# Kernel optimization log

Measured on AMD Instinct MI355X. Metric: run time of the kernel, lower is better.

The kernel has to match this reference:

```python
import jax, jax.numpy as jnp
import numpy as np

B, L, D, H = 8, 2048, 128, 128
MASK_VALUE = -1e30


def setup_inputs() -> dict:
    key = jax.random.key(0)
    ks = jax.random.split(key, 5)
    return {
        "query": jax.random.normal(ks[0], (B, L, D), dtype=jnp.float32),
        "key": jax.random.normal(ks[1], (B, L, D), dtype=jnp.float32),
        "value": jax.random.normal(ks[2], (B, L, D), dtype=jnp.float32),
        "mask": jnp.ones((B, L), dtype=jnp.float32),
        "Wq": jax.random.normal(ks[3], (D, H), dtype=jnp.float32) * (1.0 / np.sqrt(D)),
        "Wk": jax.random.normal(ks[4], (D, H), dtype=jnp.float32) * (1.0 / np.sqrt(D)),
    }


def reference(query, key, value, mask, Wq, Wk):
    # q: [B,Lq,H], k: [B,Lk,H]
    q = jnp.einsum("bqd,dh->bqh", query, Wq)
    k = jnp.einsum("bkd,dh->bkh", key, Wk)
    # unscaled scores [B,Lq,Lk]
    A = jnp.einsum("bqh,bkh->bqk", q, k)
    m = mask[:, None, :]  # [B,1,Lk]
    A = m * A + (1.0 - m) * MASK_VALUE
    # inference path: no dropout (learning_phase False)
    A = jax.nn.softmax(A, axis=-1)
    return jnp.einsum("bqk,bkd->bqd", A, value)
```

## Files before the change

kernel.cpp:

```cpp
#include <hip/hip_runtime.h>

#define NB 8
#define NL 2048
#define ND 128
#define NH 128
#define MASKVAL (-1e30f)

typedef __attribute__((ext_vector_type(8))) short short8;
typedef __attribute__((ext_vector_type(4))) float f32x4;

__device__ __forceinline__ unsigned short bf16_rn(float f) {
  unsigned u = __float_as_uint(f);
  u += 0x7fffu + ((u >> 16) & 1u);
  return (unsigned short)(u >> 16);
}
__device__ __forceinline__ float bf16_tof(unsigned short h) {
  return __uint_as_float(((unsigned)h) << 16);
}
__device__ __forceinline__ void gload16(const short* g, short* l) {
  __builtin_amdgcn_global_load_lds(
      (const __attribute__((address_space(1))) unsigned*)g,
      (__attribute__((address_space(3))) unsigned*)l, 16, 0, 0);
}


__global__ __launch_bounds__(256) void wprep_kernel(
    const float* __restrict__ Wq, const float* __restrict__ Wk,
    short* __restrict__ wthq, short* __restrict__ wtlq,
    short* __restrict__ wthk, short* __restrict__ wtlk)
{
  int m = blockIdx.x >> 4;
  int bb = blockIdx.x & 15;
  const float* W = m ? Wk : Wq;
  short* wth = m ? wthk : wthq;
  short* wtl = m ? wtlk : wtlq;
  int idx = bb * 256 + threadIdx.x;
  int d = idx >> 5, hc = idx & 31;
  float4 wv = *(const float4*)(W + d * NH + hc * 4);
  float vv[4] = {wv.x, wv.y, wv.z, wv.w};
#pragma unroll
  for (int j = 0; j < 4; ++j) {
    int h = hc * 4 + j;
    unsigned short hb = bf16_rn(vv[j]);
    unsigned short lb = bf16_rn(vv[j] - bf16_tof(hb));
    wth[h * ND + d] = (short)hb;
    wtl[h * ND + d] = (short)lb;
  }
}

__global__ __launch_bounds__(256) void vtprep_kernel(
    const float* __restrict__ value, short* __restrict__ kvs)
{
  __shared__ short Tl[64][66];
  int b = blockIdx.x >> 6;
  int k0 = ((blockIdx.x >> 1) & 31) * 64;
  int d0 = (blockIdx.x & 1) * 64;
  int t = threadIdx.x;
  int dm = t & 7, kp = t >> 3;
  float v0[8], v1[8];
  {
    const float* vp0 = value + (size_t)(b * NL + k0 + kp * 2) * ND + d0 + dm * 8;
    const float* vp1 = vp0 + ND;
    float4 a0 = *(const float4*)vp0;       float4 c0 = *(const float4*)(vp0 + 4);
    float4 a1 = *(const float4*)vp1;       float4 c1 = *(const float4*)(vp1 + 4);
    v0[0]=a0.x; v0[1]=a0.y; v0[2]=a0.z; v0[3]=a0.w; v0[4]=c0.x; v0[5]=c0.y; v0[6]=c0.z; v0[7]=c0.w;
    v1[0]=a1.x; v1[1]=a1.y; v1[2]=a1.z; v1[3]=a1.w; v1[4]=c1.x; v1[5]=c1.y; v1[6]=c1.z; v1[7]=c1.w;
  }
#pragma unroll
  for (int j = 0; j < 8; ++j) {
    unsigned pk = (unsigned)bf16_rn(v0[j]) | ((unsigned)bf16_rn(v1[j]) << 16);
    *(unsigned*)&Tl[dm * 8 + j][kp * 2] = pk;
  }
  __syncthreads();
  int dr = t >> 2, kc4 = t & 3;
  int d = d0 + dr;
  const unsigned* base = (const unsigned*)&Tl[dr][0];
  unsigned w[8];
#pragma unroll
  for (int i = 0; i < 8; ++i) w[i] = base[kc4 * 8 + i];
  int kt = (k0 >> 5) + (kc4 >> 1);
  int kcg = (kc4 & 1) * 2;
  size_t tbase = (size_t)(b * 64 + kt) * 12288 + 8192;
  int cp0 = (d * 4 + kcg) ^ (d & 7);
  int cp1 = (d * 4 + kcg + 1) ^ (d & 7);
  *(uint4*)(kvs + tbase + cp0 * 8) = make_uint4(w[0], w[1], w[2], w[3]);
  *(uint4*)(kvs + tbase + cp1 * 8) = make_uint4(w[4], w[5], w[6], w[7]);
}

__global__ __launch_bounds__(256) void proj_kernel(
    const float* __restrict__ query, const float* __restrict__ key,
    const short* __restrict__ wthq, const short* __restrict__ wtlq,
    const short* __restrict__ wthk, const short* __restrict__ wtlk,
    unsigned* __restrict__ qhl, short* __restrict__ kvs)
{
  const float* X = blockIdx.y ? key : query;
  const short* wth = blockIdx.y ? wthk : wthq;
  const short* wtl = blockIdx.y ? wtlk : wtlq;

  int tid = threadIdx.x;
  int wave = tid >> 6, lane = tid & 63;
  int lr = lane & 15, dg = lane >> 4;
  int arow = blockIdx.x * 64 + wave * 16 + lr;

  short8 ah[4], al[4];
  const float* xr = X + (size_t)arow * ND;
#pragma unroll
  for (int ks = 0; ks < 4; ++ks) {
    float4 a0 = *(const float4*)(xr + ks * 32 + dg * 8);
    float4 a1 = *(const float4*)(xr + ks * 32 + dg * 8 + 4);
    float vv[8] = {a0.x, a0.y, a0.z, a0.w, a1.x, a1.y, a1.z, a1.w};
    short8 h, l;
#pragma unroll
    for (int j = 0; j < 8; ++j) {
      unsigned short hb = bf16_rn(vv[j]);
      h[j] = (short)hb;
      l[j] = (short)bf16_rn(vv[j] - bf16_tof(hb));
    }
    ah[ks] = h; al[ks] = l;
  }

#pragma unroll
  for (int cf = 0; cf < 8; ++cf) {
    f32x4 acc = {0.f, 0.f, 0.f, 0.f};
    int col = cf * 16 + lr;
    const short* whp = wth + (size_t)col * ND;
    const short* wlp = wtl + (size_t)col * ND;
#pragma unroll
    for (int ks = 0; ks < 4; ++ks) {
      short8 wh = *(const short8*)(whp + ks * 32 + dg * 8);
      short8 wl = *(const short8*)(wlp + ks * 32 + dg * 8);
      acc = __builtin_amdgcn_mfma_f32_16x16x32_bf16(ah[ks], wh, acc, 0, 0, 0);
      acc = __builtin_amdgcn_mfma_f32_16x16x32_bf16(al[ks], wh, acc, 0, 0, 0);
      acc = __builtin_amdgcn_mfma_f32_16x16x32_bf16(ah[ks], wl, acc, 0, 0, 0);
    }
#pragma unroll
    for (int r = 0; r < 4; ++r) {
      int orow = blockIdx.x * 64 + wave * 16 + dg * 4 + r;
      float v = acc[r];
      unsigned short hb = bf16_rn(v);
      unsigned short lb = bf16_rn(v - bf16_tof(hb));
      if (blockIdx.y == 0) {
        qhl[(size_t)orow * NH + col] = ((unsigned)lb << 16) | (unsigned)hb;
      } else {
        int bb2 = orow >> 11, l2 = orow & (NL - 1);
        int kt = l2 >> 5, krow = l2 & 31;
        size_t tbase = (size_t)(bb2 * 64 + kt) * 12288;
        int gr = krow * 128 + (((col >> 3) ^ (krow & 7)) * 8) + (col & 7);
        kvs[tbase + gr] = (short)hb;
        kvs[tbase + 4096 + gr] = (short)lb;
      }
    }
  }
}

__global__ __launch_bounds__(256, 3) void attn_kernel(
    const unsigned* __restrict__ qhl, const short* __restrict__ kvs,
    const float* __restrict__ mask, float* __restrict__ out)
{
  __shared__ short KV[2][12288];
  __shared__ short Plds[4][16][32];

  int tid = threadIdx.x;
  int wave = tid >> 6, lane = tid & 63;
  int lr = lane & 15, dg = lane >> 4;
  int b = blockIdx.x & 7, qt = blockIdx.x >> 3;
  int wr = wave & 1, wk = wave >> 1;
  int q0 = qt * 32;

  short8 qh[4], ql[4];
  {
    const unsigned* qp = qhl + (size_t)(b * NL + q0 + wr * 16 + lr) * NH;
#pragma unroll
    for (int ks = 0; ks < 4; ++ks) {
      uint4 u0 = *(const uint4*)(qp + ks * 32 + dg * 8);
      uint4 u1 = *(const uint4*)(qp + ks * 32 + dg * 8 + 4);
      unsigned uv[8] = {u0.x, u0.y, u0.z, u0.w, u1.x, u1.y, u1.z, u1.w};
      short8 h, l;
#pragma unroll
      for (int j = 0; j < 8; ++j) {
        h[j] = (short)(uv[j] & 0xffffu);
        l[j] = (short)(uv[j] >> 16);
      }
      qh[ks] = h; ql[ks] = l;
    }
  }

  f32x4 accv[8];
#pragma unroll
  for (int f = 0; f < 8; ++f) accv[f] = (f32x4){0.f, 0.f, 0.f, 0.f};
  float mrow[4] = {-__builtin_inff(), -__builtin_inff(), -__builtin_inff(), -__builtin_inff()};
  float lrow[4] = {0.f, 0.f, 0.f, 0.f};

  const short* gb = kvs + (size_t)(b * 64) * 12288;
  int offbase = wr * 6144;
  const short* Kbase = &KV[wk][0];

  for (int p = 0; p < 32; ++p) {
    __syncthreads();
    {
      const short* gt = gb + (size_t)(p * 2 + wk) * 12288 + offbase + lane * 8;
      short* lt = &KV[wk][offbase];
#pragma unroll
      for (int i = 0; i < 12; ++i)
        gload16(gt + i * 512, lt + i * 512);
    }
    asm volatile("s_waitcnt vmcnt(0)" ::: "memory");
    __syncthreads();

    int kt = p * 2 + wk;
    f32x4 sc0 = {0.f, 0.f, 0.f, 0.f}, sc1 = {0.f, 0.f, 0.f, 0.f};
#pragma unroll
    for (int ks = 0; ks < 4; ++ks) {
      int chp = (((ks * 4 + dg) ^ (lr & 7)) * 8);
      short8 b0h = *(const short8*)(Kbase + lr * 128 + chp);
      short8 b0l = *(const short8*)(Kbase + 4096 + lr * 128 + chp);
      short8 b1h = *(const short8*)(Kbase + (16 + lr) * 128 + chp);
      short8 b1l = *(const short8*)(Kbase + 4096 + (16 + lr) * 128 + chp);
      sc0 = __builtin_amdgcn_mfma_f32_16x16x32_bf16(qh[ks], b0h, sc0, 0, 0, 0);
      sc1 = __builtin_amdgcn_mfma_f32_16x16x32_bf16(qh[ks], b1h, sc1, 0, 0, 0);
      sc0 = __builtin_amdgcn_mfma_f32_16x16x32_bf16(ql[ks], b0h, sc0, 0, 0, 0);
      sc1 = __builtin_amdgcn_mfma_f32_16x16x32_bf16(ql[ks], b1h, sc1, 0, 0, 0);
      sc0 = __builtin_amdgcn_mfma_f32_16x16x32_bf16(qh[ks], b0l, sc0, 0, 0, 0);
      sc1 = __builtin_amdgcn_mfma_f32_16x16x32_bf16(qh[ks], b1l, sc1, 0, 0, 0);
    }
    float mk0 = mask[b * NL + kt * 32 + lr];
    float mk1 = mask[b * NL + kt * 32 + 16 + lr];
    float pr0[4], pr1[4];
#pragma unroll
    for (int r = 0; r < 4; ++r) {
      float s0 = mk0 * sc0[r] + (1.f - mk0) * MASKVAL;
      float s1 = mk1 * sc1[r] + (1.f - mk1) * MASKVAL;
      float vmax = fmaxf(s0, s1);
      vmax = fmaxf(vmax, __shfl_xor(vmax, 1));
      vmax = fmaxf(vmax, __shfl_xor(vmax, 2));
      vmax = fmaxf(vmax, __shfl_xor(vmax, 4));
      vmax = fmaxf(vmax, __shfl_xor(vmax, 8));
      float mn = fmaxf(mrow[r], vmax);
      float alpha = __expf(mrow[r] - mn);
      float p0 = __expf(s0 - mn);
      float p1 = __expf(s1 - mn);
      float ps = p0 + p1;
      ps += __shfl_xor(ps, 1);
      ps += __shfl_xor(ps, 2);
      ps += __shfl_xor(ps, 4);
      ps += __shfl_xor(ps, 8);
      mrow[r] = mn;
      lrow[r] = lrow[r] * alpha + ps;
      pr0[r] = p0; pr1[r] = p1;
#pragma unroll
      for (int f = 0; f < 8; ++f) accv[f][r] *= alpha;
    }
#pragma unroll
    for (int r = 0; r < 4; ++r) {
      Plds[wave][dg * 4 + r][lr] = (short)bf16_rn(pr0[r]);
      Plds[wave][dg * 4 + r][16 + lr] = (short)bf16_rn(pr1[r]);
    }
    short8 pa = *(const short8*)&Plds[wave][lr][dg * 8];
#pragma unroll
    for (int f = 0; f < 8; ++f) {
      int row = f * 16 + lr;
      int cp = (((row * 4 + dg) ^ (row & 7)) * 8);
      short8 bv = *(const short8*)(Kbase + 8192 + cp);
      accv[f] = __builtin_amdgcn_mfma_f32_16x16x32_bf16(pa, bv, accv[f], 0, 0, 0);
    }
  }

  __syncthreads();
  float* obuf = (float*)&KV[0][0];
  float* mlbuf = (float*)&Plds[0][0][0];
  if (wk == 1) {
#pragma unroll
    for (int f = 0; f < 8; ++f)
#pragma unroll
      for (int r = 0; r < 4; ++r)
        obuf[(wr * 16 + dg * 4 + r) * 128 + f * 16 + lr] = accv[f][r];
    if (lr == 0) {
#pragma unroll
      for (int r = 0; r < 4; ++r) {
        mlbuf[(wr * 16 + dg * 4 + r) * 2 + 0] = mrow[r];
        mlbuf[(wr * 16 + dg * 4 + r) * 2 + 1] = lrow[r];
      }
    }
  }
  __syncthreads();
  if (wk == 0) {
#pragma unroll
    for (int r = 0; r < 4; ++r) {
      int rowl = wr * 16 + dg * 4 + r;
      float m2 = mlbuf[rowl * 2 + 0], l2 = mlbuf[rowl * 2 + 1];
      float mm = fmaxf(mrow[r], m2);
      float a1 = __expf(mrow[r] - mm), a2 = __expf(m2 - mm);
      float linv = 1.f / (a1 * lrow[r] + a2 * l2);
      int grow = b * NL + q0 + rowl;
#pragma unroll
      for (int f = 0; f < 8; ++f) {
        float o = (a1 * accv[f][r] + a2 * obuf[rowl * 128 + f * 16 + lr]) * linv;
        out[(size_t)grow * ND + f * 16 + lr] = o;
      }
    }
  }
}

extern "C" void kernel_launch(void* const* d_in, const int* in_sizes, int n_in,
                              void* d_out, int out_size, void* d_ws, size_t ws_size,
                              hipStream_t stream) {
  (void)in_sizes; (void)n_in; (void)out_size; (void)ws_size;
  const float* query = (const float*)d_in[0];
  const float* key   = (const float*)d_in[1];
  const float* value = (const float*)d_in[2];
  const float* mask  = (const float*)d_in[3];
  const float* Wq    = (const float*)d_in[4];
  const float* Wk    = (const float*)d_in[5];
  float* out = (float*)d_out;

  char* ws = (char*)d_ws;
  short* wthq = (short*)(ws);
  short* wtlq = (short*)(ws + (32 << 10));
  short* wthk = (short*)(ws + (64 << 10));
  short* wtlk = (short*)(ws + (96 << 10));
  unsigned* qhl = (unsigned*)(ws + (128 << 10));
  short* kvs = (short*)(ws + (128 << 10) + (8u << 20));

  wprep_kernel<<<dim3(32), dim3(256), 0, stream>>>(Wq, Wk, wthq, wtlq, wthk, wtlk);
  vtprep_kernel<<<dim3(512), dim3(256), 0, stream>>>(value, kvs);
  proj_kernel<<<dim3(NB * NL / 64, 2), dim3(256), 0, stream>>>(
      query, key, wthq, wtlq, wthk, wtlk, qhl, kvs);
  attn_kernel<<<dim3(NB * NL / 32), dim3(256), 0, stream>>>(qhl, kvs, mask, out);
}
```

Baseline: 183.0 us.

## Double-buffer K/V tiles, give each wave own query rows, stage stores via LDS

The attention kernel now uses 64 query rows per block, with each wave owning 16 rows across the full key range. This drops the split-K merge through shared memory. K/V tiles are double-buffered with async global-to-LDS loads, so the next tile's load overlaps the current tile's compute, and the mask row is preloaded into LDS. The projection and value-prep kernels stage their swizzled outputs in LDS and write them as coalesced 16-byte stores instead of scattered 2-byte stores. In exchange there are fewer blocks, and launch bounds now allow only one block per CU, which reduces occupancy.

```diff
diff --git a/kernel.cpp b/kernel.cpp
--- a/kernel.cpp
+++ b/kernel.cpp
@@ -17,7 +17,7 @@
 __device__ __forceinline__ float bf16_tof(unsigned short h) {
   return __uint_as_float(((unsigned)h) << 16);
 }
-__device__ __forceinline__ void gload16(const short* g, short* l) {
+__device__ __forceinline__ void gload16(const void* g, void* l) {
   __builtin_amdgcn_global_load_lds(
       (const __attribute__((address_space(1))) unsigned*)g,
       (__attribute__((address_space(3))) unsigned*)l, 16, 0, 0);
@@ -52,6 +52,7 @@
     const float* __restrict__ value, short* __restrict__ kvs)
 {
   __shared__ short Tl[64][66];
+  __shared__ short VB[2][2048];
   int b = blockIdx.x >> 6;
   int k0 = ((blockIdx.x >> 1) & 31) * 64;
   int d0 = (blockIdx.x & 1) * 64;
@@ -78,13 +79,21 @@
   unsigned w[8];
 #pragma unroll
   for (int i = 0; i < 8; ++i) w[i] = base[kc4 * 8 + i];
-  int kt = (k0 >> 5) + (kc4 >> 1);
+  int jt = kc4 >> 1;
   int kcg = (kc4 & 1) * 2;
-  size_t tbase = (size_t)(b * 64 + kt) * 12288 + 8192;
-  int cp0 = (d * 4 + kcg) ^ (d & 7);
-  int cp1 = (d * 4 + kcg + 1) ^ (d & 7);
-  *(uint4*)(kvs + tbase + cp0 * 8) = make_uint4(w[0], w[1], w[2], w[3]);
-  *(uint4*)(kvs + tbase + cp1 * 8) = make_uint4(w[4], w[5], w[6], w[7]);
+  int g0 = ((d * 4 + kcg) ^ (d & 7)) - d0 * 4;
+  int g1 = ((d * 4 + kcg + 1) ^ (d & 7)) - d0 * 4;
+  *(uint4*)&VB[jt][g0 * 8] = make_uint4(w[0], w[1], w[2], w[3]);
+  *(uint4*)&VB[jt][g1 * 8] = make_uint4(w[4], w[5], w[6], w[7]);
+  __syncthreads();
+  int kt = k0 >> 5;
+#pragma unroll
+  for (int c = 0; c < 2; ++c) {
+    int idx = c * 256 + t;
+    int j = idx >> 8, off = (idx & 255) * 8;
+    *(uint4*)(kvs + (size_t)(b * 64 + kt + j) * 12288 + 8192 + d0 * 32 + off) =
+        *(const uint4*)&VB[j][off];
+  }
 }
 
 __global__ __launch_bounds__(256) void proj_kernel(
@@ -93,6 +102,7 @@
     const short* __restrict__ wthk, const short* __restrict__ wtlk,
     unsigned* __restrict__ qhl, short* __restrict__ kvs)
 {
+  __shared__ short KB2[16384];
   const float* X = blockIdx.y ? key : query;
   const short* wth = blockIdx.y ? wthk : wthq;
   const short* wtl = blockIdx.y ? wtlk : wtlq;
@@ -142,34 +152,52 @@
       if (blockIdx.y == 0) {
         qhl[(size_t)orow * NH + col] = ((unsigned)lb << 16) | (unsigned)hb;
       } else {
-        int bb2 = orow >> 11, l2 = orow & (NL - 1);
-        int kt = l2 >> 5, krow = l2 & 31;
-        size_t tbase = (size_t)(bb2 * 64 + kt) * 12288;
+        int jj = (orow >> 5) & 1;
+        int krow = orow & 31;
         int gr = krow * 128 + (((col >> 3) ^ (krow & 7)) * 8) + (col & 7);
-        kvs[tbase + gr] = (short)hb;
-        kvs[tbase + 4096 + gr] = (short)lb;
+        KB2[jj * 8192 + gr] = (short)hb;
+        KB2[jj * 8192 + 4096 + gr] = (short)lb;
       }
     }
   }
-}
-
-__global__ __launch_bounds__(256, 3) void attn_kernel(
+  if (blockIdx.y == 1) {
+    __syncthreads();
+    int r0 = blockIdx.x * 64;
+    int bb2 = r0 >> 11;
+    int kt0 = (r0 & (NL - 1)) >> 5;
+#pragma unroll
+    for (int c = 0; c < 8; ++c) {
+      int idx = c * 256 + tid;
+      int j = idx >> 10, off = (idx & 1023) * 8;
+      *(uint4*)(kvs + (size_t)(bb2 * 64 + kt0 + j) * 12288 + off) =
+          *(const uint4*)&KB2[j * 8192 + off];
+    }
+  }
+}
+
+__global__ __launch_bounds__(256, 1) void attn_kernel(
     const unsigned* __restrict__ qhl, const short* __restrict__ kvs,
     const float* __restrict__ mask, float* __restrict__ out)
 {
   __shared__ short KV[2][12288];
+  __shared__ float Msk[NL];
   __shared__ short Plds[4][16][32];
 
   int tid = threadIdx.x;
-  int wave = tid >> 6, lane = tid & 63;
+  int w = tid >> 6, lane = tid & 63;
   int lr = lane & 15, dg = lane >> 4;
   int b = blockIdx.x & 7, qt = blockIdx.x >> 3;
-  int wr = wave & 1, wk = wave >> 1;
-  int q0 = qt * 32;
+  int q0 = qt * 64;
+
+  {
+    const float* mg = mask + b * NL + w * 512 + lane * 4;
+    gload16(mg, Msk + w * 512);
+    gload16(mg + 256, Msk + w * 512 + 256);
+  }
 
   short8 qh[4], ql[4];
   {
-    const unsigned* qp = qhl + (size_t)(b * NL + q0 + wr * 16 + lr) * NH;
+    const unsigned* qp = qhl + (size_t)(b * NL + q0 + w * 16 + lr) * NH;
 #pragma unroll
     for (int ks = 0; ks < 4; ++ks) {
       uint4 u0 = *(const uint4*)(qp + ks * 32 + dg * 8);
@@ -191,31 +219,36 @@
   float mrow[4] = {-__builtin_inff(), -__builtin_inff(), -__builtin_inff(), -__builtin_inff()};
   float lrow[4] = {0.f, 0.f, 0.f, 0.f};
 
-  const short* gb = kvs + (size_t)(b * 64) * 12288;
-  int offbase = wr * 6144;
-  const short* Kbase = &KV[wk][0];
-
-  for (int p = 0; p < 32; ++p) {
-    __syncthreads();
-    {
-      const short* gt = gb + (size_t)(p * 2 + wk) * 12288 + offbase + lane * 8;
-      short* lt = &KV[wk][offbase];
-#pragma unroll
-      for (int i = 0; i < 12; ++i)
+  const short* gbase = kvs + (size_t)(b * 64) * 12288 + w * 3072 + lane * 8;
+
+#pragma unroll
+  for (int i = 0; i < 6; ++i)
+    gload16(gbase + i * 512, &KV[0][w * 3072 + i * 512]);
+
+  for (int t = 0; t < 64; ++t) {
+    __builtin_amdgcn_s_barrier();
+    if (t + 1 < 64) {
+      const short* gt = gbase + (size_t)(t + 1) * 12288;
+      short* lt = &KV[(t + 1) & 1][w * 3072];
+#pragma unroll
+      for (int i = 0; i < 6; ++i)
         gload16(gt + i * 512, lt + i * 512);
-    }
-    asm volatile("s_waitcnt vmcnt(0)" ::: "memory");
-    __syncthreads();
-
-    int kt = p * 2 + wk;
+      asm volatile("s_waitcnt vmcnt(6)" ::: "memory");
+    } else {
+      asm volatile("s_waitcnt vmcnt(0)" ::: "memory");
+    }
+    __builtin_amdgcn_s_barrier();
+    __builtin_amdgcn_sched_barrier(0);
+
+    const short* Kb = &KV[t & 1][0];
     f32x4 sc0 = {0.f, 0.f, 0.f, 0.f}, sc1 = {0.f, 0.f, 0.f, 0.f};
 #pragma unroll
     for (int ks = 0; ks < 4; ++ks) {
       int chp = (((ks * 4 + dg) ^ (lr & 7)) * 8);
-      short8 b0h = *(const short8*)(Kbase + lr * 128 + chp);
-      short8 b0l = *(const short8*)(Kbase + 4096 + lr * 128 + chp);
-      short8 b1h = *(const short8*)(Kbase + (16 + lr) * 128 + chp);
-      short8 b1l = *(const short8*)(Kbase + 4096 + (16 + lr) * 128 + chp);
+      short8 b0h = *(const short8*)(Kb + lr * 128 + chp);
+      short8 b0l = *(const short8*)(Kb + 4096 + lr * 128 + chp);
+      short8 b1h = *(const short8*)(Kb + (16 + lr) * 128 + chp);
+      short8 b1l = *(const short8*)(Kb + 4096 + (16 + lr) * 128 + chp);
       sc0 = __builtin_amdgcn_mfma_f32_16x16x32_bf16(qh[ks], b0h, sc0, 0, 0, 0);
       sc1 = __builtin_amdgcn_mfma_f32_16x16x32_bf16(qh[ks], b1h, sc1, 0, 0, 0);
       sc0 = __builtin_amdgcn_mfma_f32_16x16x32_bf16(ql[ks], b0h, sc0, 0, 0, 0);
@@ -223,8 +256,8 @@
       sc0 = __builtin_amdgcn_mfma_f32_16x16x32_bf16(qh[ks], b0l, sc0, 0, 0, 0);
       sc1 = __builtin_amdgcn_mfma_f32_16x16x32_bf16(qh[ks], b1l, sc1, 0, 0, 0);
     }
-    float mk0 = mask[b * NL + kt * 32 + lr];
-    float mk1 = mask[b * NL + kt * 32 + 16 + lr];
+    float mk0 = Msk[t * 32 + lr];
+    float mk1 = Msk[t * 32 + 16 + lr];
     float pr0[4], pr1[4];
 #pragma unroll
     for (int r = 0; r < 4; ++r) {
@@ -252,52 +285,26 @@
     }
 #pragma unroll
     for (int r = 0; r < 4; ++r) {
-      Plds[wave][dg * 4 + r][lr] = (short)bf16_rn(pr0[r]);
-      Plds[wave][dg * 4 + r][16 + lr] = (short)bf16_rn(pr1[r]);
-    }
-    short8 pa = *(const short8*)&Plds[wave][lr][dg * 8];
+      Plds[w][dg * 4 + r][lr] = (short)bf16_rn(pr0[r]);
+      Plds[w][dg * 4 + r][16 + lr] = (short)bf16_rn(pr1[r]);
+    }
+    short8 pa = *(const short8*)&Plds[w][lr][dg * 8];
 #pragma unroll
     for (int f = 0; f < 8; ++f) {
       int row = f * 16 + lr;
       int cp = (((row * 4 + dg) ^ (row & 7)) * 8);
-      short8 bv = *(const short8*)(Kbase + 8192 + cp);
+      short8 bv = *(const short8*)(Kb + 8192 + cp);
       accv[f] = __builtin_amdgcn_mfma_f32_16x16x32_bf16(pa, bv, accv[f], 0, 0, 0);
     }
   }
 
-  __syncthreads();
-  float* obuf = (float*)&KV[0][0];
-  float* mlbuf = (float*)&Plds[0][0][0];
-  if (wk == 1) {
+#pragma unroll
+  for (int r = 0; r < 4; ++r) {
+    float linv = 1.f / lrow[r];
+    int grow = b * NL + q0 + w * 16 + dg * 4 + r;
 #pragma unroll
     for (int f = 0; f < 8; ++f)
-#pragma unroll
-      for (int r = 0; r < 4; ++r)
-        obuf[(wr * 16 + dg * 4 + r) * 128 + f * 16 + lr] = accv[f][r];
-    if (lr == 0) {
-#pragma unroll
-      for (int r = 0; r < 4; ++r) {
-        mlbuf[(wr * 16 + dg * 4 + r) * 2 + 0] = mrow[r];
-        mlbuf[(wr * 16 + dg * 4 + r) * 2 + 1] = lrow[r];
-      }
-    }
-  }
-  __syncthreads();
-  if (wk == 0) {
-#pragma unroll
-    for (int r = 0; r < 4; ++r) {
-      int rowl = wr * 16 + dg * 4 + r;
-      float m2 = mlbuf[rowl * 2 + 0], l2 = mlbuf[rowl * 2 + 1];
-      float mm = fmaxf(mrow[r], m2);
-      float a1 = __expf(mrow[r] - mm), a2 = __expf(m2 - mm);
-      float linv = 1.f / (a1 * lrow[r] + a2 * l2);
-      int grow = b * NL + q0 + rowl;
-#pragma unroll
-      for (int f = 0; f < 8; ++f) {
-        float o = (a1 * accv[f][r] + a2 * obuf[rowl * 128 + f * 16 + lr]) * linv;
-        out[(size_t)grow * ND + f * 16 + lr] = o;
-      }
-    }
+      out[(size_t)grow * ND + f * 16 + lr] = accv[f][r] * linv;
   }
 }
 
@@ -325,5 +332,5 @@
   vtprep_kernel<<<dim3(512), dim3(256), 0, stream>>>(value, kvs);
   proj_kernel<<<dim3(NB * NL / 64, 2), dim3(256), 0, stream>>>(
       query, key, wthq, wtlq, wthk, wtlk, qhl, kvs);
-  attn_kernel<<<dim3(NB * NL / 32), dim3(256), 0, stream>>>(qhl, kvs, mask, out);
-}
+  attn_kernel<<<dim3(NB * NL / 64), dim3(256), 0, stream>>>(qhl, kvs, mask, out);
+}
```

Measured after the change: 209.6 us. +14.6%, slower.
